# Performance work log

Hardware: AMD Instinct MI355X
Metric: run time of the kernel (lower is better)

## Reference

```python
import jax, jax.numpy as jnp
from jax import lax
import numpy as np

N_IN = 4          # n_in_channels (WN input); coupling input has 2*N_IN channels
N_CTX = 80        # n_context_channels
N_LAYERS = 8
N_CH = 256        # n_channels (must be even)
K = 3             # kernel_size (odd)
DILATIONS = [1, 2, 4, 8, 16, 32, 64, 128]
B, T = 8, 4096


def conv1d(x, w, b, dilation=1):
    # x: [B, Cin, T], w: [Cout, Cin, K], 'same' padding as in the torch module
    pad = (w.shape[-1] * dilation - dilation) // 2
    y = lax.conv_general_dilated(
        x, w, window_strides=(1,), padding=[(pad, pad)],
        rhs_dilation=(dilation,), dimension_numbers=('NCH', 'OIH', 'NCH'))
    return y + b[None, :, None]


def setup_inputs() -> dict:
    key = jax.random.key(0)
    ks = jax.random.split(key, 14)
    s = 0.05  # weight scale to keep exp(log_s) well-conditioned
    inp = {
        'forecast': jax.random.normal(ks[0], (B, 2 * N_IN, T), jnp.float32),
        'context':  jax.random.normal(ks[1], (B, N_CTX, T), jnp.float32),
        'start_w': jax.random.normal(ks[2], (N_CH, N_IN, 1), jnp.float32) * s,
        'start_b': jax.random.normal(ks[3], (N_CH,), jnp.float32) * s,
        'cond_w':  jax.random.normal(ks[4], (2 * N_CH * N_LAYERS, N_CTX, 1), jnp.float32) * s,
        'cond_b':  jax.random.normal(ks[5], (2 * N_CH * N_LAYERS,), jnp.float32) * s,
        'in_w':    jax.random.normal(ks[6], (N_LAYERS, 2 * N_CH, N_CH, K), jnp.float32) * s,
        'in_b':    jax.random.normal(ks[7], (N_LAYERS, 2 * N_CH), jnp.float32) * s,
        # res_skip: layers 0..L-2 have 2*N_CH out channels; last layer uses only first N_CH
        'rs_w':    jax.random.normal(ks[8], (N_LAYERS, 2 * N_CH, N_CH, 1), jnp.float32) * s,
        'rs_b':    jax.random.normal(ks[9], (N_LAYERS, 2 * N_CH), jnp.float32) * s,
        'end_w':   jax.random.normal(ks[10], (2 * N_IN, N_CH, 1), jnp.float32) * 0.01,
        'end_b':   jax.random.normal(ks[11], (2 * N_IN,), jnp.float32) * 0.01,
    }
    return inp


def wn(f0, context, start_w, start_b, cond_w, cond_b, in_w, in_b, rs_w, rs_b, end_w, end_b):
    x = conv1d(f0, start_w, start_b)                 # [B, N_CH, T]
    ctx = conv1d(context, cond_w, cond_b)            # [B, 2*N_CH*L, T]
    output = jnp.zeros_like(x)
    for i in range(N_LAYERS):
        a = conv1d(x, in_w[i], in_b[i], DILATIONS[i])
        a = a + ctx[:, i * 2 * N_CH:(i + 1) * 2 * N_CH, :]
        acts = jnp.tanh(a[:, :N_CH, :]) * jax.nn.sigmoid(a[:, N_CH:, :])
        if i < N_LAYERS - 1:
            rs = conv1d(acts, rs_w[i], rs_b[i])      # [B, 2*N_CH, T]
            x = x + rs[:, :N_CH, :]
            output = output + rs[:, N_CH:, :]
        else:
            rs = conv1d(acts, rs_w[i][:N_CH], rs_b[i][:N_CH])
            output = output + rs
    return conv1d(output, end_w, end_b)              # [B, 2*N_IN, T]


def reference(forecast, context, start_w, start_b, cond_w, cond_b,
              in_w, in_b, rs_w, rs_b, end_w, end_b):
    n_half = forecast.shape[1] // 2
    f0 = forecast[:, :n_half, :]
    f1 = forecast[:, n_half:, :]
    out = wn(f0, context, start_w, start_b, cond_w, cond_b,
             in_w, in_b, rs_w, rs_b, end_w, end_b)
    log_s = out[:, n_half:, :]
    b = out[:, :n_half, :]
    f1 = jnp.exp(log_s) * f1 + b
    return jnp.concatenate([f0, f1], axis=1), log_s
```

## Files before the change

### kernel.cpp

```cpp
#include <hip/hip_runtime.h>

#define BATCH 8
#define T 4096
#define NCH 256
#define NCTX 80
#define NLAYERS 8

typedef unsigned short u16;
typedef __attribute__((ext_vector_type(8))) short short8;
typedef __attribute__((ext_vector_type(4))) short short4v;
typedef __attribute__((ext_vector_type(4))) float float4v;

__device__ __forceinline__ float b2f(u16 u) {
    unsigned v = ((unsigned)u) << 16;
    float f;
    __builtin_memcpy(&f, &v, 4);
    return f;
}
__device__ __forceinline__ u16 f2b(float f) {
    unsigned v;
    __builtin_memcpy(&v, &f, 4);
    unsigned r = v + 0x7FFFu + ((v >> 16) & 1u);
    return (u16)(r >> 16);
}

typedef const __attribute__((address_space(1))) unsigned int* gp1;
typedef __attribute__((address_space(3))) unsigned int* lp3;
__device__ __forceinline__ void gl_lds16(const u16* g, u16* l) {
    __builtin_amdgcn_global_load_lds((gp1)g, (lp3)l, 16, 0, 0);
}

__device__ __forceinline__ void wb0() { asm volatile("s_waitcnt vmcnt(0) lgkmcnt(0)\n\ts_barrier" ::: "memory"); }
__device__ __forceinline__ void wb4() { asm volatile("s_waitcnt vmcnt(4) lgkmcnt(0)\n\ts_barrier" ::: "memory"); }
__device__ __forceinline__ void wb5() { asm volatile("s_waitcnt vmcnt(5) lgkmcnt(0)\n\ts_barrier" ::: "memory"); }

template <bool F32>
__device__ __forceinline__ float LD(const void* p, size_t i) {
    if constexpr (F32) return ((const float*)p)[i];
    else return b2f(((const u16*)p)[i]);
}

__global__ void probe_kernel(const u16* __restrict__ fc, int* __restrict__ flag) {
    __shared__ int cnt;
    if (threadIdx.x == 0) cnt = 0;
    __syncthreads();
    int local = 0;
#pragma unroll
    for (int j = 0; j < 16; j++) {
        u16 u = fc[2 * (threadIdx.x * 16 + j)];
        int e = (u >> 7) & 0xFF;
        if (e >= 0x50 && e <= 0x85) local++;
    }
    atomicAdd(&cnt, local);
    __syncthreads();
    if (threadIdx.x == 0) *flag = (cnt >= 2048) ? 1 : 0;
}

__global__ void cvt_kernel(const void* __restrict__ src, u16* __restrict__ dst, int n,
                           const int* __restrict__ flag) {
    int i = blockIdx.x * 256 + threadIdx.x;
    if (i >= n) return;
    if (*flag) dst[i] = f2b(LD<false>(src, i));
    else       dst[i] = f2b(LD<true>(src, i));
}

template <bool F32>
__device__ __forceinline__ void prep_wc_body(const void* __restrict__ in_w,
                                             const void* __restrict__ in_b,
                                             const void* __restrict__ cond_w,
                                             const void* __restrict__ cond_b,
                                             u16* __restrict__ Wc) {
    int row = blockIdx.x;
    for (int it = 0; it < 4; it++) {
        int col = it * 256 + threadIdx.x;
        if (col >= 864) break;
        float v;
        if (col < 256)       v = LD<F32>(in_w, ((size_t)row * 256 + col) * 3);
        else if (col < 512)  v = LD<F32>(in_w, ((size_t)row * 256 + (col - 256)) * 3 + 1);
        else if (col < 768)  v = LD<F32>(in_w, ((size_t)row * 256 + (col - 512)) * 3 + 2);
        else if (col < 848)  v = LD<F32>(cond_w, (size_t)row * 80 + (col - 768));
        else if (col == 848) v = LD<F32>(in_b, row) + LD<F32>(cond_b, row);
        else                 v = 0.f;
        Wc[(size_t)row * 864 + col] = f2b(v);
    }
}
__global__ void prep_wc(const void* __restrict__ in_w, const void* __restrict__ in_b,
                        const void* __restrict__ cond_w, const void* __restrict__ cond_b,
                        u16* __restrict__ Wc, const int* __restrict__ flag) {
    if (*flag) prep_wc_body<false>(in_w, in_b, cond_w, cond_b, Wc);
    else       prep_wc_body<true>(in_w, in_b, cond_w, cond_b, Wc);
}

template <bool F32>
__device__ __forceinline__ void prep_ctx_body(const void* __restrict__ ctx,
                                              u16* __restrict__ ctxt, float (*sm)[65]) {
    const int tid = threadIdx.x;
    const int b = blockIdx.y, t0 = blockIdx.x * 64;
    for (int it = 0; it < 20; it++) {
        int e = it * 256 + tid;
        int j = e >> 6, tt = e & 63;
        sm[j][tt] = LD<F32>(ctx, ((size_t)b * 80 + j) * T + t0 + tt);
    }
    __syncthreads();
    for (int it = 0; it < 24; it++) {
        int e = it * 256 + tid;
        int r = e / 96, c = e - r * 96;
        float v = (c < 80) ? sm[c][r] : (c == 80 ? 1.f : 0.f);
        ctxt[((size_t)b * T + t0 + r) * 96 + c] = f2b(v);
    }
}
__global__ void prep_ctx(const void* __restrict__ ctx, u16* __restrict__ ctxt,
                         const int* __restrict__ flag) {
    __shared__ float sm[80][65];
    if (*flag) prep_ctx_body<false>(ctx, ctxt, sm);
    else       prep_ctx_body<true>(ctx, ctxt, sm);
}

template <bool F32>
__device__ __forceinline__ void start_body(const void* __restrict__ fc,
                                           const void* __restrict__ w,
                                           const void* __restrict__ bias,
                                           u16* __restrict__ xt, float (*fsm)[64],
                                           float* wsm, float* bsm) {
    const int tid = threadIdx.x;
    const int b = blockIdx.y, t0 = blockIdx.x * 64;
    fsm[tid >> 6][tid & 63] = LD<F32>(fc, ((size_t)b * 8 + (tid >> 6)) * T + t0 + (tid & 63));
    for (int it = 0; it < 4; it++) wsm[it * 256 + tid] = LD<F32>(w, it * 256 + tid);
    bsm[tid] = LD<F32>(bias, tid);
    __syncthreads();
    for (int r = 0; r < 64; r++) {
        int c = tid;
        float a = bsm[c];
#pragma unroll
        for (int k = 0; k < 4; k++) a += wsm[c * 4 + k] * fsm[k][r];
        xt[((size_t)b * T + t0 + r) * 256 + c] = f2b(a);
    }
}
__global__ void start_kernel(const void* __restrict__ fc, const void* __restrict__ w,
                             const void* __restrict__ bias, u16* __restrict__ xt,
                             const int* __restrict__ flag) {
    __shared__ float fsm[4][64];
    __shared__ float wsm[1024];
    __shared__ float bsm[256];
    if (*flag) start_body<false>(fc, w, bias, xt, fsm, wsm, bsm);
    else       start_body<true>(fc, w, bias, xt, fsm, wsm, bsm);
}

__global__ __launch_bounds__(512, 1) void layer_conv(
    const u16* __restrict__ x, const u16* __restrict__ Wc, const u16* __restrict__ ctxt,
    u16* __restrict__ acts, int layer, int dil) {
    __shared__ u16 lds[61440];
    const int tid = threadIdx.x;
    const int w = tid >> 6, lane = tid & 63;
    const int l15 = lane & 15, quad = lane >> 4;
    const int iw = w >> 2, jc = w & 3;
    const int b = blockIdx.y, t0 = blockIdx.x * 128;
    const int lrow = lane >> 2;
    const int fw = (lrow ^ (lrow >> 2)) & 3;
    const int lsw = ((lane & 3) ^ fw) * 8;
    const int fr = (l15 ^ (l15 >> 2)) & 3;
    const int rq = (quad ^ fr) * 8;
    const int brb = 64 * (w >> 1) + 256 * (w & 1);

    const u16* xb = x + (size_t)b * T * 256;
    const u16* cb = ctxt + (size_t)b * T * 96;
    const u16* Wl = Wc + (size_t)layer * 512 * 864;

    float4v acc[4][8];
#pragma unroll
    for (int m = 0; m < 4; m++)
#pragma unroll
        for (int jj = 0; jj < 8; jj++) acc[m][jj] = (float4v){0.f, 0.f, 0.f, 0.f};

    auto stageA = [&](int s, int abuf) -> int {
        u16* dst = &lds[abuf * 4096 + w * 512];
        if (s < 24) {
            int seg = s >> 3, cs = s & 7;
            int tb = t0 + 16 * w + (seg - 1) * dil;
            if (tb >= 0 && tb + 16 <= T) {
                gl_lds16(xb + (size_t)(tb + lrow) * 256 + cs * 32 + lsw, dst);
                return 1;
            } else {
                int t = tb + lrow;
                short8 av = (short8){0, 0, 0, 0, 0, 0, 0, 0};
                if (t >= 0 && t < T)
                    av = *(const short8*)(xb + (size_t)t * 256 + cs * 32 + lsw);
                *(short4v*)&dst[lane * 8] = __builtin_shufflevector(av, av, 0, 1, 2, 3);
                *(short4v*)&dst[lane * 8 + 4] = __builtin_shufflevector(av, av, 4, 5, 6, 7);
                return 0;
            }
        } else {
            gl_lds16(cb + (size_t)(t0 + 16 * w + lrow) * 96 + (s - 24) * 32 + lsw, dst);
            return 1;
        }
    };
    auto stageB = [&](int s, int bbuf) {
        const u16* src = Wl + (size_t)(brb + lrow) * 864 + s * 32 + lsw;
        u16* dst = &lds[12288 + bbuf * 16384 + w * 2048];
        gl_lds16(src, dst);
        gl_lds16(src + (size_t)16 * 864, dst + 512);
        gl_lds16(src + (size_t)32 * 864, dst + 1024);
        gl_lds16(src + (size_t)48 * 864, dst + 1536);
    };

    int a0 = stageA(0, 0);
    stageB(0, 0);
    int a1 = stageA(1, 1);
    stageB(1, 1);
    (void)a0;
    if (a1) wb5(); else wb4();
#pragma unroll 1
    for (int s = 0; s < 27; s++) {
        int aiss = 0;
        if (s + 2 < 27) {
            aiss = stageA(s + 2, (s + 2) % 3);
            stageB(s + 2, (s + 2) % 3);
        }
        const u16* bA = &lds[(s % 3) * 4096];
        const u16* bB = &lds[12288 + (s % 3) * 16384];
        short8 af0 = *(const short8*)&bA[(64 * iw + l15) * 32 + rq];
        short8 af1 = *(const short8*)&bA[(64 * iw + 16 + l15) * 32 + rq];
        short8 af2 = *(const short8*)&bA[(64 * iw + 32 + l15) * 32 + rq];
        short8 af3 = *(const short8*)&bA[(64 * iw + 48 + l15) * 32 + rq];
        __builtin_amdgcn_s_setprio(1);
#pragma unroll
        for (int jj = 0; jj < 8; jj++) {
            short8 bf = *(const short8*)&bB[(128 * jc + 16 * jj + l15) * 32 + rq];
            acc[0][jj] = __builtin_amdgcn_mfma_f32_16x16x32_bf16(af0, bf, acc[0][jj], 0, 0, 0);
            acc[1][jj] = __builtin_amdgcn_mfma_f32_16x16x32_bf16(af1, bf, acc[1][jj], 0, 0, 0);
            acc[2][jj] = __builtin_amdgcn_mfma_f32_16x16x32_bf16(af2, bf, acc[2][jj], 0, 0, 0);
            acc[3][jj] = __builtin_amdgcn_mfma_f32_16x16x32_bf16(af3, bf, acc[3][jj], 0, 0, 0);
        }
        __builtin_amdgcn_s_setprio(0);
        if (s < 25) {
            if (aiss) wb5(); else wb4();
        } else if (s == 25) {
            wb0();
        }
    }

    u16* ab = acts + (size_t)b * T * 256;
#pragma unroll
    for (int m = 0; m < 4; m++)
#pragma unroll
        for (int jj = 0; jj < 4; jj++) {
            int o = 64 * jc + 16 * jj + l15;
#pragma unroll
            for (int r = 0; r < 4; r++) {
                int t = t0 + 64 * iw + 16 * m + quad * 4 + r;
                float at = acc[m][jj][r], as = acc[m][jj + 4][r];
                float e2 = __expf(2.f * at);
                float th = 1.f - 2.f / (e2 + 1.f);
                float sg = 1.f / (1.f + __expf(-as));
                ab[(size_t)t * 256 + o] = f2b(th * sg);
            }
        }
}

__global__ __launch_bounds__(512, 1) void layer_rs(
    const u16* __restrict__ acts, u16* __restrict__ x, const u16* __restrict__ Wrs,
    const u16* __restrict__ rsb, u16* __restrict__ oacc, int layer, int first, int last) {
    __shared__ u16 lds[61440];
    const int tid = threadIdx.x;
    const int w = tid >> 6, lane = tid & 63;
    const int l15 = lane & 15, quad = lane >> 4;
    const int iw = w >> 2, jc = w & 3;
    const int b = blockIdx.y, t0 = blockIdx.x * 128;
    const int lrow = lane >> 2;
    const int fw = (lrow ^ (lrow >> 2)) & 3;
    const int lsw = ((lane & 3) ^ fw) * 8;
    const int fr = (l15 ^ (l15 >> 2)) & 3;
    const int rq = (quad ^ fr) * 8;
    const int brb = 64 * (w >> 1) + 256 * (w & 1);

    const u16* ab = acts + (size_t)b * T * 256;
    const u16* Wr = Wrs + (size_t)layer * 512 * 256;

    float4v acc[4][8];
#pragma unroll
    for (int m = 0; m < 4; m++)
#pragma unroll
        for (int jj = 0; jj < 8; jj++) acc[m][jj] = (float4v){0.f, 0.f, 0.f, 0.f};

    auto stageA = [&](int s, int abuf) {
        gl_lds16(ab + (size_t)(t0 + 16 * w + lrow) * 256 + s * 32 + lsw,
                 &lds[abuf * 4096 + w * 512]);
    };
    auto stageB = [&](int s, int bbuf) {
        const u16* src = Wr + (size_t)(brb + lrow) * 256 + s * 32 + lsw;
        u16* dst = &lds[12288 + bbuf * 16384 + w * 2048];
        gl_lds16(src, dst);
        gl_lds16(src + (size_t)16 * 256, dst + 512);
        gl_lds16(src + (size_t)32 * 256, dst + 1024);
        gl_lds16(src + (size_t)48 * 256, dst + 1536);
    };

    stageA(0, 0);
    stageB(0, 0);
    stageA(1, 1);
    stageB(1, 1);
    wb5();
#pragma unroll 1
    for (int s = 0; s < 8; s++) {
        if (s + 2 < 8) {
            stageA(s + 2, (s + 2) % 3);
            stageB(s + 2, (s + 2) % 3);
        }
        const u16* bA = &lds[(s % 3) * 4096];
        const u16* bB = &lds[12288 + (s % 3) * 16384];
        short8 af0 = *(const short8*)&bA[(64 * iw + l15) * 32 + rq];
        short8 af1 = *(const short8*)&bA[(64 * iw + 16 + l15) * 32 + rq];
        short8 af2 = *(const short8*)&bA[(64 * iw + 32 + l15) * 32 + rq];
        short8 af3 = *(const short8*)&bA[(64 * iw + 48 + l15) * 32 + rq];
        __builtin_amdgcn_s_setprio(1);
#pragma unroll
        for (int jj = 0; jj < 8; jj++) {
            short8 bf = *(const short8*)&bB[(128 * jc + 16 * jj + l15) * 32 + rq];
            acc[0][jj] = __builtin_amdgcn_mfma_f32_16x16x32_bf16(af0, bf, acc[0][jj], 0, 0, 0);
            acc[1][jj] = __builtin_amdgcn_mfma_f32_16x16x32_bf16(af1, bf, acc[1][jj], 0, 0, 0);
            acc[2][jj] = __builtin_amdgcn_mfma_f32_16x16x32_bf16(af2, bf, acc[2][jj], 0, 0, 0);
            acc[3][jj] = __builtin_amdgcn_mfma_f32_16x16x32_bf16(af3, bf, acc[3][jj], 0, 0, 0);
        }
        __builtin_amdgcn_s_setprio(0);
        if (s < 6) wb5();
        else if (s == 6) wb0();
    }

    u16* xv = x + (size_t)b * T * 256;
    u16* oo = oacc + (size_t)b * T * 256;
#pragma unroll
    for (int m = 0; m < 4; m++)
#pragma unroll
        for (int jj = 0; jj < 8; jj++) {
            int o = 64 * jc + 16 * (jj & 3) + l15;
            if (jj < 4) {
                float b0 = b2f(rsb[layer * 512 + o]);
#pragma unroll
                for (int r = 0; r < 4; r++) {
                    int t = t0 + 64 * iw + 16 * m + quad * 4 + r;
                    size_t idx = (size_t)t * 256 + o;
                    float v0 = acc[m][jj][r] + b0;
                    if (last) oo[idx] = f2b(b2f(oo[idx]) + v0);
                    else      xv[idx] = f2b(b2f(xv[idx]) + v0);
                }
            } else if (!last) {
                float b1 = b2f(rsb[layer * 512 + 256 + o]);
#pragma unroll
                for (int r = 0; r < 4; r++) {
                    int t = t0 + 64 * iw + 16 * m + quad * 4 + r;
                    size_t idx = (size_t)t * 256 + o;
                    float v1 = acc[m][jj][r] + b1;
                    oo[idx] = first ? f2b(v1) : f2b(b2f(oo[idx]) + v1);
                }
            }
        }
}

template <bool F32>
__device__ __forceinline__ void end_body(const u16* __restrict__ oacc,
                                         const void* __restrict__ w_end,
                                         const void* __restrict__ b_end,
                                         const void* __restrict__ fc, void* __restrict__ out,
                                         float* wsm, float* bsm) {
    const int tid = threadIdx.x;
    for (int it = 0; it < 8; it++) wsm[it * 256 + tid] = LD<F32>(w_end, it * 256 + tid);
    if (tid < 8) bsm[tid] = LD<F32>(b_end, tid);
    __syncthreads();
    int gid = blockIdx.x * 256 + tid;
    int b = gid >> 12, t = gid & 4095;
    float o8[8];
#pragma unroll
    for (int o = 0; o < 8; o++) o8[o] = bsm[o];
    const u16* orow = oacc + (size_t)(b * T + t) * 256;
    for (int c8 = 0; c8 < 32; c8++) {
        short8 v8 = *(const short8*)(orow + c8 * 8);
#pragma unroll
        for (int k = 0; k < 8; k++) {
            float v = b2f((u16)v8[k]);
            int c = c8 * 8 + k;
#pragma unroll
            for (int o = 0; o < 8; o++) o8[o] += wsm[o * 256 + c] * v;
        }
    }
    size_t ob8 = (size_t)b * 8 * T;
#pragma unroll
    for (int j = 0; j < 4; j++) {
        float f1v = LD<F32>(fc, ob8 + (size_t)(4 + j) * T + t);
        float ls = o8[4 + j];
        float val = __expf(ls) * f1v + o8[j];
        if constexpr (F32) {
            float* o = (float*)out;
            o[ob8 + (size_t)j * T + t] = ((const float*)fc)[ob8 + (size_t)j * T + t];
            o[ob8 + (size_t)(4 + j) * T + t] = val;
            o[(size_t)BATCH * 8 * T + ((size_t)b * 4 + j) * T + t] = ls;
        } else {
            u16* o = (u16*)out;
            o[ob8 + (size_t)j * T + t] = ((const u16*)fc)[ob8 + (size_t)j * T + t];
            o[ob8 + (size_t)(4 + j) * T + t] = f2b(val);
            o[(size_t)BATCH * 8 * T + ((size_t)b * 4 + j) * T + t] = f2b(ls);
        }
    }
}
__global__ void end_kernel(const u16* __restrict__ oacc, const void* __restrict__ w_end,
                           const void* __restrict__ b_end, const void* __restrict__ fc,
                           void* __restrict__ out, const int* __restrict__ flag) {
    __shared__ float wsm[2048];
    __shared__ float bsm[8];
    if (*flag) end_body<false>(oacc, w_end, b_end, fc, out, wsm, bsm);
    else       end_body<true>(oacc, w_end, b_end, fc, out, wsm, bsm);
}

extern "C" void kernel_launch(void* const* d_in, const int* in_sizes, int n_in,
                              void* d_out, int out_size, void* d_ws, size_t ws_size,
                              hipStream_t stream) {
    const void* forecast = d_in[0];
    const void* context  = d_in[1];
    const void* start_w  = d_in[2];
    const void* start_b  = d_in[3];
    const void* cond_w   = d_in[4];
    const void* cond_b   = d_in[5];
    const void* in_w     = d_in[6];
    const void* in_b     = d_in[7];
    const void* rs_w     = d_in[8];
    const void* rs_b     = d_in[9];
    const void* end_w    = d_in[10];
    const void* end_b    = d_in[11];

    char* W = (char*)d_ws;
    int* flag = (int*)(W + 0);
    u16* xA   = (u16*)(W + 256);
    u16* oacc = (u16*)(W + 256 + 16777216);
    u16* acts = (u16*)(W + 256 + 33554432);
    u16* ctxt = (u16*)(W + 256 + 50331648);
    u16* Wc   = (u16*)(W + 256 + 56623104);
    u16* Wrs  = (u16*)(W + 256 + 63700992);
    u16* rsb  = (u16*)(W + 256 + 65798144);

    probe_kernel<<<1, 256, 0, stream>>>((const u16*)forecast, flag);

    cvt_kernel<<<4096, 256, 0, stream>>>(rs_w, Wrs, 8 * 512 * 256, flag);
    cvt_kernel<<<16, 256, 0, stream>>>(rs_b, rsb, 4096, flag);
    prep_wc<<<4096, 256, 0, stream>>>(in_w, in_b, cond_w, cond_b, Wc, flag);
    prep_ctx<<<dim3(64, BATCH), 256, 0, stream>>>(context, ctxt, flag);
    start_kernel<<<dim3(64, BATCH), 256, 0, stream>>>(forecast, start_w, start_b, xA, flag);

    const int dil[NLAYERS] = {1, 2, 4, 8, 16, 32, 64, 128};
    for (int l = 0; l < NLAYERS; l++) {
        layer_conv<<<dim3(32, BATCH), 512, 0, stream>>>(xA, Wc, ctxt, acts, l, dil[l]);
        layer_rs<<<dim3(32, BATCH), 512, 0, stream>>>(acts, xA, Wrs, rsb, oacc, l,
                                                      l == 0, l == NLAYERS - 1);
    }

    end_kernel<<<128, 256, 0, stream>>>(oacc, end_w, end_b, forecast, d_out, flag);
}
```

Before: 672.0 us.

## Halve time tile per block and switch to double-buffered pipeline

Shrinks each block's time tile from 128 to 64 rows, doubling the grid to 512 blocks so all CUs get work (previously 256 blocks on a 256-CU part with one block each). LDS drops from 3-stage to 2-stage buffering, only half the waves load the A tile, and accumulators halve, which allows higher launch-bound occupancy. The cost is that weight tiles are re-streamed twice as often per time step, and the single-stage prefetch waits on all loads (vmcnt(0)) every iteration.

```diff
diff --git a/kernel.cpp b/kernel.cpp
--- a/kernel.cpp
+++ b/kernel.cpp
@@ -30,9 +30,7 @@
     __builtin_amdgcn_global_load_lds((gp1)g, (lp3)l, 16, 0, 0);
 }
 
-__device__ __forceinline__ void wb0() { asm volatile("s_waitcnt vmcnt(0) lgkmcnt(0)\n\ts_barrier" ::: "memory"); }
-__device__ __forceinline__ void wb4() { asm volatile("s_waitcnt vmcnt(4) lgkmcnt(0)\n\ts_barrier" ::: "memory"); }
-__device__ __forceinline__ void wb5() { asm volatile("s_waitcnt vmcnt(5) lgkmcnt(0)\n\ts_barrier" ::: "memory"); }
+__device__ __forceinline__ void wbar() { asm volatile("s_waitcnt vmcnt(0) lgkmcnt(0)\n\ts_barrier" ::: "memory"); }
 
 template <bool F32>
 __device__ __forceinline__ float LD(const void* p, size_t i) {
@@ -146,15 +144,15 @@
     else       start_body<true>(fc, w, bias, xt, fsm, wsm, bsm);
 }
 
-__global__ __launch_bounds__(512, 1) void layer_conv(
+__global__ __launch_bounds__(512, 4) void layer_conv(
     const u16* __restrict__ x, const u16* __restrict__ Wc, const u16* __restrict__ ctxt,
     u16* __restrict__ acts, int layer, int dil) {
-    __shared__ u16 lds[61440];
+    __shared__ u16 lds[36864];
     const int tid = threadIdx.x;
     const int w = tid >> 6, lane = tid & 63;
     const int l15 = lane & 15, quad = lane >> 4;
     const int iw = w >> 2, jc = w & 3;
-    const int b = blockIdx.y, t0 = blockIdx.x * 128;
+    const int b = blockIdx.y, t0 = blockIdx.x * 64;
     const int lrow = lane >> 2;
     const int fw = (lrow ^ (lrow >> 2)) & 3;
     const int lsw = ((lane & 3) ^ fw) * 8;
@@ -166,20 +164,20 @@
     const u16* cb = ctxt + (size_t)b * T * 96;
     const u16* Wl = Wc + (size_t)layer * 512 * 864;
 
-    float4v acc[4][8];
-#pragma unroll
-    for (int m = 0; m < 4; m++)
+    float4v acc[2][8];
+#pragma unroll
+    for (int m = 0; m < 2; m++)
 #pragma unroll
         for (int jj = 0; jj < 8; jj++) acc[m][jj] = (float4v){0.f, 0.f, 0.f, 0.f};
 
-    auto stageA = [&](int s, int abuf) -> int {
-        u16* dst = &lds[abuf * 4096 + w * 512];
+    auto stageA = [&](int s, int abuf) {
+        if (w >= 4) return;
+        u16* dst = &lds[abuf * 2048 + w * 512];
         if (s < 24) {
             int seg = s >> 3, cs = s & 7;
             int tb = t0 + 16 * w + (seg - 1) * dil;
             if (tb >= 0 && tb + 16 <= T) {
                 gl_lds16(xb + (size_t)(tb + lrow) * 256 + cs * 32 + lsw, dst);
-                return 1;
             } else {
                 int t = tb + lrow;
                 short8 av = (short8){0, 0, 0, 0, 0, 0, 0, 0};
@@ -187,67 +185,56 @@
                     av = *(const short8*)(xb + (size_t)t * 256 + cs * 32 + lsw);
                 *(short4v*)&dst[lane * 8] = __builtin_shufflevector(av, av, 0, 1, 2, 3);
                 *(short4v*)&dst[lane * 8 + 4] = __builtin_shufflevector(av, av, 4, 5, 6, 7);
-                return 0;
             }
         } else {
             gl_lds16(cb + (size_t)(t0 + 16 * w + lrow) * 96 + (s - 24) * 32 + lsw, dst);
-            return 1;
         }
     };
     auto stageB = [&](int s, int bbuf) {
         const u16* src = Wl + (size_t)(brb + lrow) * 864 + s * 32 + lsw;
-        u16* dst = &lds[12288 + bbuf * 16384 + w * 2048];
+        u16* dst = &lds[4096 + bbuf * 16384 + w * 2048];
         gl_lds16(src, dst);
         gl_lds16(src + (size_t)16 * 864, dst + 512);
         gl_lds16(src + (size_t)32 * 864, dst + 1024);
         gl_lds16(src + (size_t)48 * 864, dst + 1536);
     };
-
-    int a0 = stageA(0, 0);
-    stageB(0, 0);
-    int a1 = stageA(1, 1);
-    stageB(1, 1);
-    (void)a0;
-    if (a1) wb5(); else wb4();
-#pragma unroll 1
-    for (int s = 0; s < 27; s++) {
-        int aiss = 0;
-        if (s + 2 < 27) {
-            aiss = stageA(s + 2, (s + 2) % 3);
-            stageB(s + 2, (s + 2) % 3);
-        }
-        const u16* bA = &lds[(s % 3) * 4096];
-        const u16* bB = &lds[12288 + (s % 3) * 16384];
-        short8 af0 = *(const short8*)&bA[(64 * iw + l15) * 32 + rq];
-        short8 af1 = *(const short8*)&bA[(64 * iw + 16 + l15) * 32 + rq];
-        short8 af2 = *(const short8*)&bA[(64 * iw + 32 + l15) * 32 + rq];
-        short8 af3 = *(const short8*)&bA[(64 * iw + 48 + l15) * 32 + rq];
+    auto compute = [&](int s) {
+        const u16* bA = &lds[(s & 1) * 2048];
+        const u16* bB = &lds[4096 + (s & 1) * 16384];
+        short8 af0 = *(const short8*)&bA[(32 * iw + l15) * 32 + rq];
+        short8 af1 = *(const short8*)&bA[(32 * iw + 16 + l15) * 32 + rq];
         __builtin_amdgcn_s_setprio(1);
 #pragma unroll
         for (int jj = 0; jj < 8; jj++) {
             short8 bf = *(const short8*)&bB[(128 * jc + 16 * jj + l15) * 32 + rq];
             acc[0][jj] = __builtin_amdgcn_mfma_f32_16x16x32_bf16(af0, bf, acc[0][jj], 0, 0, 0);
             acc[1][jj] = __builtin_amdgcn_mfma_f32_16x16x32_bf16(af1, bf, acc[1][jj], 0, 0, 0);
-            acc[2][jj] = __builtin_amdgcn_mfma_f32_16x16x32_bf16(af2, bf, acc[2][jj], 0, 0, 0);
-            acc[3][jj] = __builtin_amdgcn_mfma_f32_16x16x32_bf16(af3, bf, acc[3][jj], 0, 0, 0);
         }
         __builtin_amdgcn_s_setprio(0);
-        if (s < 25) {
-            if (aiss) wb5(); else wb4();
-        } else if (s == 25) {
-            wb0();
-        }
+    };
+
+    stageA(0, 0);
+    stageB(0, 0);
+    wbar();
+#pragma unroll 1
+    for (int s = 0; s < 27; s++) {
+        if (s + 1 < 27) {
+            stageA(s + 1, (s + 1) & 1);
+            stageB(s + 1, (s + 1) & 1);
+        }
+        compute(s);
+        if (s + 1 < 27) wbar();
     }
 
     u16* ab = acts + (size_t)b * T * 256;
 #pragma unroll
-    for (int m = 0; m < 4; m++)
+    for (int m = 0; m < 2; m++)
 #pragma unroll
         for (int jj = 0; jj < 4; jj++) {
             int o = 64 * jc + 16 * jj + l15;
 #pragma unroll
             for (int r = 0; r < 4; r++) {
-                int t = t0 + 64 * iw + 16 * m + quad * 4 + r;
+                int t = t0 + 32 * iw + 16 * m + quad * 4 + r;
                 float at = acc[m][jj][r], as = acc[m][jj + 4][r];
                 float e2 = __expf(2.f * at);
                 float th = 1.f - 2.f / (e2 + 1.f);
@@ -257,15 +244,15 @@
         }
 }
 
-__global__ __launch_bounds__(512, 1) void layer_rs(
+__global__ __launch_bounds__(512, 4) void layer_rs(
     const u16* __restrict__ acts, u16* __restrict__ x, const u16* __restrict__ Wrs,
     const u16* __restrict__ rsb, u16* __restrict__ oacc, int layer, int first, int last) {
-    __shared__ u16 lds[61440];
+    __shared__ u16 lds[36864];
     const int tid = threadIdx.x;
     const int w = tid >> 6, lane = tid & 63;
     const int l15 = lane & 15, quad = lane >> 4;
     const int iw = w >> 2, jc = w & 3;
-    const int b = blockIdx.y, t0 = blockIdx.x * 128;
+    const int b = blockIdx.y, t0 = blockIdx.x * 64;
     const int lrow = lane >> 2;
     const int fw = (lrow ^ (lrow >> 2)) & 3;
     const int lsw = ((lane & 3) ^ fw) * 8;
@@ -276,60 +263,57 @@
     const u16* ab = acts + (size_t)b * T * 256;
     const u16* Wr = Wrs + (size_t)layer * 512 * 256;
 
-    float4v acc[4][8];
-#pragma unroll
-    for (int m = 0; m < 4; m++)
+    float4v acc[2][8];
+#pragma unroll
+    for (int m = 0; m < 2; m++)
 #pragma unroll
         for (int jj = 0; jj < 8; jj++) acc[m][jj] = (float4v){0.f, 0.f, 0.f, 0.f};
 
     auto stageA = [&](int s, int abuf) {
+        if (w >= 4) return;
         gl_lds16(ab + (size_t)(t0 + 16 * w + lrow) * 256 + s * 32 + lsw,
-                 &lds[abuf * 4096 + w * 512]);
+                 &lds[abuf * 2048 + w * 512]);
     };
     auto stageB = [&](int s, int bbuf) {
         const u16* src = Wr + (size_t)(brb + lrow) * 256 + s * 32 + lsw;
-        u16* dst = &lds[12288 + bbuf * 16384 + w * 2048];
+        u16* dst = &lds[4096 + bbuf * 16384 + w * 2048];
         gl_lds16(src, dst);
         gl_lds16(src + (size_t)16 * 256, dst + 512);
         gl_lds16(src + (size_t)32 * 256, dst + 1024);
         gl_lds16(src + (size_t)48 * 256, dst + 1536);
     };
-
-    stageA(0, 0);
-    stageB(0, 0);
-    stageA(1, 1);
-    stageB(1, 1);
-    wb5();
-#pragma unroll 1
-    for (int s = 0; s < 8; s++) {
-        if (s + 2 < 8) {
-            stageA(s + 2, (s + 2) % 3);
-            stageB(s + 2, (s + 2) % 3);
-        }
-        const u16* bA = &lds[(s % 3) * 4096];
-        const u16* bB = &lds[12288 + (s % 3) * 16384];
-        short8 af0 = *(const short8*)&bA[(64 * iw + l15) * 32 + rq];
-        short8 af1 = *(const short8*)&bA[(64 * iw + 16 + l15) * 32 + rq];
-        short8 af2 = *(const short8*)&bA[(64 * iw + 32 + l15) * 32 + rq];
-        short8 af3 = *(const short8*)&bA[(64 * iw + 48 + l15) * 32 + rq];
+    auto compute = [&](int s) {
+        const u16* bA = &lds[(s & 1) * 2048];
+        const u16* bB = &lds[4096 + (s & 1) * 16384];
+        short8 af0 = *(const short8*)&bA[(32 * iw + l15) * 32 + rq];
+        short8 af1 = *(const short8*)&bA[(32 * iw + 16 + l15) * 32 + rq];
         __builtin_amdgcn_s_setprio(1);
 #pragma unroll
         for (int jj = 0; jj < 8; jj++) {
             short8 bf = *(const short8*)&bB[(128 * jc + 16 * jj + l15) * 32 + rq];
             acc[0][jj] = __builtin_amdgcn_mfma_f32_16x16x32_bf16(af0, bf, acc[0][jj], 0, 0, 0);
             acc[1][jj] = __builtin_amdgcn_mfma_f32_16x16x32_bf16(af1, bf, acc[1][jj], 0, 0, 0);
-            acc[2][jj] = __builtin_amdgcn_mfma_f32_16x16x32_bf16(af2, bf, acc[2][jj], 0, 0, 0);
-            acc[3][jj] = __builtin_amdgcn_mfma_f32_16x16x32_bf16(af3, bf, acc[3][jj], 0, 0, 0);
         }
         __builtin_amdgcn_s_setprio(0);
-        if (s < 6) wb5();
-        else if (s == 6) wb0();
+    };
+
+    stageA(0, 0);
+    stageB(0, 0);
+    wbar();
+#pragma unroll 1
+    for (int s = 0; s < 8; s++) {
+        if (s + 1 < 8) {
+            stageA(s + 1, (s + 1) & 1);
+            stageB(s + 1, (s + 1) & 1);
+        }
+        compute(s);
+        if (s + 1 < 8) wbar();
     }
 
     u16* xv = x + (size_t)b * T * 256;
     u16* oo = oacc + (size_t)b * T * 256;
 #pragma unroll
-    for (int m = 0; m < 4; m++)
+    for (int m = 0; m < 2; m++)
 #pragma unroll
         for (int jj = 0; jj < 8; jj++) {
             int o = 64 * jc + 16 * (jj & 3) + l15;
@@ -337,7 +321,7 @@
                 float b0 = b2f(rsb[layer * 512 + o]);
 #pragma unroll
                 for (int r = 0; r < 4; r++) {
-                    int t = t0 + 64 * iw + 16 * m + quad * 4 + r;
+                    int t = t0 + 32 * iw + 16 * m + quad * 4 + r;
                     size_t idx = (size_t)t * 256 + o;
                     float v0 = acc[m][jj][r] + b0;
                     if (last) oo[idx] = f2b(b2f(oo[idx]) + v0);
@@ -347,7 +331,7 @@
                 float b1 = b2f(rsb[layer * 512 + 256 + o]);
 #pragma unroll
                 for (int r = 0; r < 4; r++) {
-                    int t = t0 + 64 * iw + 16 * m + quad * 4 + r;
+                    int t = t0 + 32 * iw + 16 * m + quad * 4 + r;
                     size_t idx = (size_t)t * 256 + o;
                     float v1 = acc[m][jj][r] + b1;
                     oo[idx] = first ? f2b(v1) : f2b(b2f(oo[idx]) + v1);
@@ -446,8 +430,8 @@
 
     const int dil[NLAYERS] = {1, 2, 4, 8, 16, 32, 64, 128};
     for (int l = 0; l < NLAYERS; l++) {
-        layer_conv<<<dim3(32, BATCH), 512, 0, stream>>>(xA, Wc, ctxt, acts, l, dil[l]);
-        layer_rs<<<dim3(32, BATCH), 512, 0, stream>>>(acts, xA, Wrs, rsb, oacc, l,
+        layer_conv<<<dim3(64, BATCH), 512, 0, stream>>>(xA, Wc, ctxt, acts, l, dil[l]);
+        layer_rs<<<dim3(64, BATCH), 512, 0, stream>>>(acts, xA, Wrs, rsb, oacc, l,
                                                       l == 0, l == NLAYERS - 1);
     }
 
```

New measurement: 700.5 us. +4.2%, slower.
